# Kernel tuning notes

Hardware: AMD Instinct MI355X
Metric: run time of the kernel (lower is better)

## Reference

```python
import jax, jax.numpy as jnp
import numpy as np


def _segment_mean(x, idx, num_segments):
    # mean-aggregate rows of x into num_segments buckets (PyG SAGEConv default aggr)
    s = jax.ops.segment_sum(x, idx, num_segments=num_segments)
    c = jax.ops.segment_sum(jnp.ones((idx.shape[0],), x.dtype), idx, num_segments=num_segments)
    return s / jnp.maximum(c, 1.0)[:, None]


def setup_inputs() -> dict:
    key = jax.random.key(0)
    ks = jax.random.split(key, 12)
    N_LIG, N_PROT, D, H, E = 100000, 50000, 64, 128, 2000000
    sc = 0.05
    return {
        "x_lig": jax.random.normal(ks[0], (N_LIG, D), jnp.float32),
        "x_prot": jax.random.normal(ks[1], (N_PROT, D), jnp.float32),
        "W_l_lp": jax.random.normal(ks[2], (D, H), jnp.float32) * sc,
        "b_lp": jnp.zeros((H,), jnp.float32),
        "W_r_lp": jax.random.normal(ks[3], (D, H), jnp.float32) * sc,
        "W_l_pl": jax.random.normal(ks[4], (D, H), jnp.float32) * sc,
        "b_pl": jnp.zeros((H,), jnp.float32),
        "W_r_pl": jax.random.normal(ks[5], (D, H), jnp.float32) * sc,
        "W_lin": jax.random.normal(ks[6], (H, 1), jnp.float32) * sc,
        "b_lin": jnp.zeros((1,), jnp.float32),
        "src_lp": jax.random.randint(ks[7], (E,), 0, N_LIG, jnp.int32),
        "dst_lp": jax.random.randint(ks[8], (E,), 0, N_PROT, jnp.int32),
        "src_pl": jax.random.randint(ks[9], (E,), 0, N_PROT, jnp.int32),
        "dst_pl": jax.random.randint(ks[10], (E,), 0, N_LIG, jnp.int32),
    }


def reference(x_lig, x_prot, W_l_lp, b_lp, W_r_lp, W_l_pl, b_pl, W_r_pl,
              W_lin, b_lin, src_lp, dst_lp, src_pl, dst_pl):
    n_lig = x_lig.shape[0]
    n_prot = x_prot.shape[0]
    # SAGEConv ('ligand','interacts','protein'): gather ligand feats along edges, mean into proteins
    agg_prot = _segment_mean(x_lig[src_lp], dst_lp, n_prot)          # [N_prot, D]
    h_prot = jax.nn.relu(agg_prot @ W_l_lp + b_lp + x_prot @ W_r_lp)  # [N_prot, H] (dead downstream, as in original)
    # SAGEConv ('protein','interacts','ligand')
    agg_lig = _segment_mean(x_prot[src_pl], dst_pl, n_lig)           # [N_lig, D]
    h_lig = jax.nn.relu(agg_lig @ W_l_pl + b_pl + x_lig @ W_r_pl)    # [N_lig, H]
    ligand_out = h_lig.mean(axis=0)                                  # [H]
    del h_prot  # original computes it but never uses it (only 'ligand' feeds the head)
    return ligand_out @ W_lin + b_lin                                # [1]
```

## Files before the change

### kernel.cpp

```cpp
#include <hip/hip_runtime.h>

#define D 64
#define H 128
#define BN 128
#define CAP 3456
#define NBB 256
#define CE 7816

typedef short bf16x8 __attribute__((ext_vector_type(8)));
typedef float f32x4  __attribute__((ext_vector_type(4)));
typedef float f32x2  __attribute__((ext_vector_type(2)));

__device__ __forceinline__ ushort f2bf(float f) {
    unsigned u = __float_as_uint(f);
    unsigned r = (u + 0x7FFFu + ((u >> 16) & 1u)) >> 16;
    return (ushort)r;
}

__device__ __forceinline__ bf16x8 pack8v(f32x4 a, f32x4 b) {
    ushort o[8];
    o[0]=f2bf(a[0]); o[1]=f2bf(a[1]); o[2]=f2bf(a[2]); o[3]=f2bf(a[3]);
    o[4]=f2bf(b[0]); o[5]=f2bf(b[1]); o[6]=f2bf(b[2]); o[7]=f2bf(b[3]);
    bf16x8 r;
    __builtin_memcpy(&r, o, 16);
    return r;
}

__device__ __forceinline__ void acc16(f32x2* a, uint4 v) {
    a[0] += __builtin_amdgcn_cvt_pk_f32_fp8((int)v.x, false);
    a[1] += __builtin_amdgcn_cvt_pk_f32_fp8((int)v.x, true);
    a[2] += __builtin_amdgcn_cvt_pk_f32_fp8((int)v.y, false);
    a[3] += __builtin_amdgcn_cvt_pk_f32_fp8((int)v.y, true);
    a[4] += __builtin_amdgcn_cvt_pk_f32_fp8((int)v.z, false);
    a[5] += __builtin_amdgcn_cvt_pk_f32_fp8((int)v.z, true);
    a[6] += __builtin_amdgcn_cvt_pk_f32_fp8((int)v.w, false);
    a[7] += __builtin_amdgcn_cvt_pk_f32_fp8((int)v.w, true);
}

__device__ __forceinline__ unsigned pk4_fp8(float x0, float x1, float x2, float x3) {
    int w = __builtin_amdgcn_cvt_pk_fp8_f32(x0, x1, 0, false);
    w = __builtin_amdgcn_cvt_pk_fp8_f32(x2, x3, w, true);
    return (unsigned)w;
}

__device__ __forceinline__ int wave_incl_scan(int v, int lane) {
    #pragma unroll
    for (int o = 1; o < 64; o <<= 1) {
        int x = __shfl_up(v, o);
        if (lane >= o) v += x;
    }
    return v;
}

__global__ __launch_bounds__(256)
void stage1_kernel(const float* __restrict__ xp, unsigned char* __restrict__ xp8, int totalp,
                   const float* __restrict__ Wl, const float* __restrict__ Wr,
                   ushort* __restrict__ wprep,
                   const int* __restrict__ dst, int* __restrict__ cnt,
                   int E, int K, int ce, int PB) {
    __shared__ int scnt[800];
    int bid = blockIdx.x;
    int t = threadIdx.x;
    if (bid < PB) {
        int i = (bid * 256 + t) * 16;
        if (i < totalp) {
            const f32x4* p = (const f32x4*)(xp + i);
            f32x4 a = __builtin_nontemporal_load(p);
            f32x4 b = __builtin_nontemporal_load(p + 1);
            f32x4 c = __builtin_nontemporal_load(p + 2);
            f32x4 d = __builtin_nontemporal_load(p + 3);
            uint4 o;
            o.x = pk4_fp8(a[0], a[1], a[2], a[3]);
            o.y = pk4_fp8(b[0], b[1], b[2], b[3]);
            o.z = pk4_fp8(c[0], c[1], c[2], c[3]);
            o.w = pk4_fp8(d[0], d[1], d[2], d[3]);
            *(uint4*)(xp8 + i) = o;
        }
    } else if (bid < PB + 8) {
        int e = (bid - PB) * 256 + t;
        if (e < 2048) {
            int lane = e & 63;
            int ks = (e >> 6) & 3;
            int ht = e >> 8;
            int h = ht * 16 + (lane & 15);
            int kgp = lane >> 4;
            ushort o[8];
            #pragma unroll
            for (int j = 0; j < 8; ++j) {
                int k = (ks < 2) ? (kgp * 16 + ks * 8 + j)
                                 : (ks * 32 + kgp * 8 + j);
                float v = (k < D) ? Wl[k * H + h] : Wr[(k - D) * H + h];
                o[j] = f2bf(v);
            }
            *(bf16x8*)(wprep + (size_t)e * 8) = *(bf16x8*)o;
        }
    } else {
        int blk = bid - PB - 8;
        for (int b = t; b < 800; b += 256) scnt[b] = 0;
        __syncthreads();
        int e0 = blk * ce;
        int e1 = min(E, e0 + ce);
        for (int i = e0 + t * 4; i < e1; i += 1024) {
            int4 d4 = *(const int4*)(dst + i);
            atomicAdd(&scnt[d4.x >> 7], 1);
            atomicAdd(&scnt[d4.y >> 7], 1);
            atomicAdd(&scnt[d4.z >> 7], 1);
            atomicAdd(&scnt[d4.w >> 7], 1);
        }
        __syncthreads();
        int* row = cnt + (size_t)blk * K;
        for (int b = t; b < K; b += 256) row[b] = scnt[b];
    }
}

__global__ __launch_bounds__(NBB)
void part_scan_kernel(const int* __restrict__ cnt, int* __restrict__ off,
                      int* __restrict__ tot, int K) {
    __shared__ int wsum[NBB / 64];
    int b = blockIdx.x;
    int t = threadIdx.x;
    int lane = t & 63, wv = t >> 6;
    int v = cnt[(size_t)t * K + b];
    int incl = wave_incl_scan(v, lane);
    if (lane == 63) wsum[wv] = incl;
    __syncthreads();
    int add = 0;
    #pragma unroll
    for (int w = 0; w < NBB / 64; ++w)
        if (w < wv) add += wsum[w];
    off[(size_t)t * K + b] = incl + add - v;
    if (t == NBB - 1) tot[b] = incl + add;
}

__global__ __launch_bounds__(512)
void part_scatter_kernel(const int* __restrict__ src, const int* __restrict__ dst,
                         const int* __restrict__ off, int* __restrict__ gb,
                         int E, int K, int ce) {
    __shared__ int shist[800];
    __shared__ int sbase[800];
    __shared__ int gdelta[800];
    __shared__ int lcur[800];
    __shared__ int sscan[512];
    __shared__ int ebuf[CE];
    __shared__ unsigned short bkt[CE];

    int blk = blockIdx.x, t = threadIdx.x;
    int e0 = blk * ce;
    int e1 = min(E, e0 + ce);
    int myn = e1 - e0;

    int4 dreg[4];
    #pragma unroll
    for (int k = 0; k < 4; ++k) {
        int i = e0 + (t + k * 512) * 4;
        dreg[k] = (i < e1) ? *(const int4*)(dst + i) : make_int4(-1, -1, -1, -1);
    }

    for (int b = t; b < 800; b += 512) shist[b] = 0;
    __syncthreads();
    #pragma unroll
    for (int k = 0; k < 4; ++k) {
        if (dreg[k].x >= 0) {
            atomicAdd(&shist[dreg[k].x >> 7], 1);
            atomicAdd(&shist[dreg[k].y >> 7], 1);
            atomicAdd(&shist[dreg[k].z >> 7], 1);
            atomicAdd(&shist[dreg[k].w >> 7], 1);
        }
    }
    __syncthreads();
    int c0 = 0, c1 = 0;
    if (t < 400) { c0 = shist[2 * t]; c1 = shist[2 * t + 1]; }
    int cs = c0 + c1;
    sscan[t] = (t < 400) ? cs : 0;
    __syncthreads();
    for (int o = 1; o < 512; o <<= 1) {
        int x = (t >= o) ? sscan[t - o] : 0;
        __syncthreads();
        sscan[t] += x;
        __syncthreads();
    }
    if (t < 400) {
        int ex = sscan[t] - cs;
        sbase[2 * t] = ex;
        sbase[2 * t + 1] = ex + c0;
    }
    __syncthreads();
    const int* orow = off + (size_t)blk * K;
    for (int b = t; b < K; b += 512) {
        int sb = sbase[b];
        gdelta[b] = orow[b] - sb;
        lcur[b] = sb;
    }
    __syncthreads();
    #pragma unroll
    for (int k = 0; k < 4; ++k) {
        int i = e0 + (t + k * 512) * 4;
        if (dreg[k].x >= 0) {
            int4 s4 = *(const int4*)(src + i);
            int b, p;
            b = dreg[k].x >> 7; p = atomicAdd(&lcur[b], 1);
            ebuf[p] = (s4.x & 0xFFFF) | ((dreg[k].x & 127) << 16); bkt[p] = (unsigned short)b;
            b = dreg[k].y >> 7; p = atomicAdd(&lcur[b], 1);
            ebuf[p] = (s4.y & 0xFFFF) | ((dreg[k].y & 127) << 16); bkt[p] = (unsigned short)b;
            b = dreg[k].z >> 7; p = atomicAdd(&lcur[b], 1);
            ebuf[p] = (s4.z & 0xFFFF) | ((dreg[k].z & 127) << 16); bkt[p] = (unsigned short)b;
            b = dreg[k].w >> 7; p = atomicAdd(&lcur[b], 1);
            ebuf[p] = (s4.w & 0xFFFF) | ((dreg[k].w & 127) << 16); bkt[p] = (unsigned short)b;
        }
    }
    __syncthreads();
    for (int p = t; p < myn; p += 512) {
        int b = bkt[p];
        int loc = gdelta[b] + p;
        if (loc < CAP) gb[(size_t)b * CAP + loc] = ebuf[p];
    }
}

__global__ __launch_bounds__(512, 6)
void fused_kernel(const unsigned char* __restrict__ xp8, const float* __restrict__ x_lig,
                  const int* __restrict__ gtot, const int* __restrict__ gb,
                  const ushort* __restrict__ wprep, const float* __restrict__ bvec,
                  float* __restrict__ pgrid, int N) {
    __shared__ int sdeg[BN];
    __shared__ int sstart[BN];
    __shared__ int scur[BN];
    __shared__ int swtot[2];
    __shared__ int scsr[CAP];
    __shared__ float sred[8][H];

    int b = blockIdx.x, t = threadIdx.x;
    int wv = t >> 6, lane = t & 63;
    int cnt = min(gtot[b], CAP);
    const int* mygb = gb + (size_t)b * CAP;

    int ev[7];
    #pragma unroll
    for (int k = 0; k < 7; ++k) {
        int i = t + k * 512;
        ev[k] = (i < cnt) ? __builtin_nontemporal_load(&mygb[i]) : -1;
    }

    if (t < BN) sdeg[t] = 0;
    __syncthreads();
    #pragma unroll
    for (int k = 0; k < 7; ++k)
        if (ev[k] >= 0) atomicAdd(&sdeg[ev[k] >> 16], 1);
    __syncthreads();
    int degv = 0, inclv = 0;
    if (t < BN) {
        degv = sdeg[t];
        inclv = wave_incl_scan(degv, lane);
        if (lane == 63) swtot[wv] = inclv;
    }
    __syncthreads();
    if (t < BN) {
        int ex = inclv + ((t >= 64) ? swtot[0] : 0) - degv;
        sstart[t] = ex;
        scur[t] = ex;
    }
    __syncthreads();
    #pragma unroll
    for (int k = 0; k < 7; ++k)
        if (ev[k] >= 0) {
            int p = atomicAdd(&scur[ev[k] >> 16], 1);
            scsr[p] = ev[k] & 0xFFFF;
        }
    __syncthreads();

    int r = lane & 15, kg = lane >> 4;

    int grow = b * BN + wv * 16 + r;
    f32x4 va = {0.f,0.f,0.f,0.f}, vb = va, vc = va, vd = va;
    if (grow < N) {
        const f32x4* xr = (const f32x4*)(x_lig + (size_t)grow * D);
        va = __builtin_nontemporal_load(xr + kg * 2);
        vb = __builtin_nontemporal_load(xr + kg * 2 + 1);
        vc = __builtin_nontemporal_load(xr + 8 + kg * 2);
        vd = __builtin_nontemporal_load(xr + 8 + kg * 2 + 1);
    }

    int ln = wv * 16 + r;
    int s0 = sstart[ln], dg = sdeg[ln];
    f32x2 a[8];
    #pragma unroll
    for (int k = 0; k < 8; ++k) { a[k][0] = 0.f; a[k][1] = 0.f; }
    int j = 0;
    for (; j + 1 < dg; j += 2) {
        int i0 = scsr[s0 + j];
        int i1 = scsr[s0 + j + 1];
        uint4 v0 = *((const uint4*)(xp8 + (size_t)i0 * D) + kg);
        uint4 v1 = *((const uint4*)(xp8 + (size_t)i1 * D) + kg);
        acc16(a, v0);
        acc16(a, v1);
    }
    if (j < dg) {
        int i0 = scsr[s0 + j];
        uint4 v0 = *((const uint4*)(xp8 + (size_t)i0 * D) + kg);
        acc16(a, v0);
    }

    float inv = 1.0f / fmaxf((float)dg, 1.0f);
    ushort o0[8], o1[8];
    #pragma unroll
    for (int k = 0; k < 4; ++k) {
        o0[2*k]   = f2bf(a[k][0] * inv);
        o0[2*k+1] = f2bf(a[k][1] * inv);
        o1[2*k]   = f2bf(a[4+k][0] * inv);
        o1[2*k+1] = f2bf(a[4+k][1] * inv);
    }
    bf16x8 A0, A1;
    __builtin_memcpy(&A0, o0, 16);
    __builtin_memcpy(&A1, o1, 16);

    bf16x8 A2 = pack8v(va, vb);
    bf16x8 A3 = pack8v(vc, vd);

    float hsum[8];
    bool full = (b * BN + wv * 16 + 16 <= N);
    const bf16x8* wp = (const bf16x8*)wprep;
    #pragma unroll 2
    for (int ht = 0; ht < 8; ++ht) {
        f32x4 acc = {0.f, 0.f, 0.f, 0.f};
        acc = __builtin_amdgcn_mfma_f32_16x16x32_bf16(A0, wp[(ht*4+0)*64 + lane], acc, 0, 0, 0);
        acc = __builtin_amdgcn_mfma_f32_16x16x32_bf16(A1, wp[(ht*4+1)*64 + lane], acc, 0, 0, 0);
        acc = __builtin_amdgcn_mfma_f32_16x16x32_bf16(A2, wp[(ht*4+2)*64 + lane], acc, 0, 0, 0);
        acc = __builtin_amdgcn_mfma_f32_16x16x32_bf16(A3, wp[(ht*4+3)*64 + lane], acc, 0, 0, 0);
        float bb = bvec[ht * 16 + r];
        float s = 0.f;
        if (full) {
            #pragma unroll
            for (int i = 0; i < 4; ++i) s += fmaxf(acc[i] + bb, 0.f);
        } else {
            #pragma unroll
            for (int i = 0; i < 4; ++i) {
                int row = b * BN + wv * 16 + kg * 4 + i;
                if (row < N) s += fmaxf(acc[i] + bb, 0.f);
            }
        }
        hsum[ht] = s;
    }

    #pragma unroll
    for (int ht = 0; ht < 8; ++ht) {
        float v = hsum[ht];
        v += __shfl_xor(v, 16);
        v += __shfl_xor(v, 32);
        if (lane < 16) sred[wv][ht * 16 + lane] = v;
    }
    __syncthreads();
    if (t < H) {
        float s = 0.f;
        #pragma unroll
        for (int w = 0; w < 8; ++w) s += sred[w][t];
        pgrid[(size_t)b * H + t] = s;
    }
}

__global__ __launch_bounds__(128)
void reduce1_kernel(const float* __restrict__ pgrid, int nb, float* __restrict__ pgrid2) {
    int t = threadIdx.x;
    float s = 0.f;
    for (int r = blockIdx.x; r < nb; r += 64) s += pgrid[(size_t)r * H + t];
    pgrid2[(size_t)blockIdx.x * H + t] = s;
}

__global__ __launch_bounds__(128)
void head_kernel(const float* __restrict__ pgrid2,
                 const float* __restrict__ W_lin, const float* __restrict__ b_lin,
                 float* __restrict__ out, float invN) {
    __shared__ float sh[H];
    int t = threadIdx.x;
    float s = 0.f;
    #pragma unroll 8
    for (int r = 0; r < 64; ++r) s += pgrid2[(size_t)r * H + t];
    sh[t] = s * invN * W_lin[t];
    __syncthreads();
    if (t == 0) {
        float tot = b_lin[0];
        for (int i = 0; i < H; ++i) tot += sh[i];
        out[0] = tot;
    }
}

extern "C" void kernel_launch(void* const* d_in, const int* in_sizes, int n_in,
                              void* d_out, int out_size, void* d_ws, size_t ws_size,
                              hipStream_t stream) {
    const float* x_lig  = (const float*)d_in[0];
    const float* x_prot = (const float*)d_in[1];
    const float* W_l_pl = (const float*)d_in[5];
    const float* b_pl   = (const float*)d_in[6];
    const float* W_r_pl = (const float*)d_in[7];
    const float* W_lin  = (const float*)d_in[8];
    const float* b_lin  = (const float*)d_in[9];
    const int*   src_pl = (const int*)d_in[12];
    const int*   dst_pl = (const int*)d_in[13];

    int N  = in_sizes[0] / D;
    int NP = in_sizes[1] / D;
    int E  = in_sizes[12];
    int K  = (N + BN - 1) / BN;

    char* base = (char*)d_ws;
    unsigned char* xp8 = (unsigned char*)base; base += (size_t)NP * D;
    float* pgrid  = (float*)base;   base += (size_t)K * H * sizeof(float);
    float* pgrid2 = (float*)base;   base += (size_t)64 * H * sizeof(float);
    ushort* wprep = (ushort*)base;  base += (size_t)2048 * 8 * sizeof(ushort);
    int* cnt      = (int*)base;     base += (size_t)NBB * K * sizeof(int);
    int* off      = (int*)base;     base += (size_t)NBB * K * sizeof(int);
    int* tot      = (int*)base;     base += (size_t)K * sizeof(int);
    base = (char*)(((size_t)base + 255) & ~(size_t)255);
    int* gb       = (int*)base;     base += (size_t)K * CAP * sizeof(int);

    int ce = ((E + NBB - 1) / NBB + 3) & ~3;
    int PB = (NP * D / 16 + 255) / 256;

    stage1_kernel<<<PB + 8 + NBB, 256, 0, stream>>>(x_prot, xp8, NP * D,
                                                    W_l_pl, W_r_pl, wprep,
                                                    dst_pl, cnt, E, K, ce, PB);
    part_scan_kernel<<<K, NBB, 0, stream>>>(cnt, off, tot, K);
    part_scatter_kernel<<<NBB, 512, 0, stream>>>(src_pl, dst_pl, off, gb, E, K, ce);
    fused_kernel<<<K, 512, 0, stream>>>(xp8, x_lig, tot, gb, wprep, b_pl, pgrid, N);
    reduce1_kernel<<<64, 128, 0, stream>>>(pgrid, K, pgrid2);
    head_kernel<<<1, 128, 0, stream>>>(pgrid2, W_lin, b_lin, (float*)d_out,
                                       1.0f / (float)N);
}
```

Before: 79.26 us.

## Sort nodes by degree within block and stage weights in LDS

Each block computes a rank of its 128 destination nodes by in-degree and remaps the rows so each wave's 16 lanes handle nodes of similar degree, which reduces divergence in the gather loop. The prepacked weight fragments are also copied into shared memory once per block and read from LDS in the MFMA loop instead of global memory. The cost is an O(BN) rank loop per thread, an extra 32KB of LDS that may lower occupancy, and a row mask for tail handling.

```diff
diff --git a/kernel.cpp b/kernel.cpp
--- a/kernel.cpp
+++ b/kernel.cpp
@@ -225,14 +225,24 @@
     __shared__ int sstart[BN];
     __shared__ int scur[BN];
     __shared__ int swtot[2];
+    __shared__ int slot[BN];
     __shared__ int scsr[CAP];
     __shared__ float sred[8][H];
+    __shared__ ushort swp[2048 * 8];
 
     int b = blockIdx.x, t = threadIdx.x;
     int wv = t >> 6, lane = t & 63;
     int cnt = min(gtot[b], CAP);
     const int* mygb = gb + (size_t)b * CAP;
 
+    {
+        const uint4* wsrc = (const uint4*)wprep;
+        uint4* wdst = (uint4*)swp;
+        #pragma unroll
+        for (int k = 0; k < 4; ++k)
+            wdst[t + k * 512] = wsrc[t + k * 512];
+    }
+
     int ev[7];
     #pragma unroll
     for (int k = 0; k < 7; ++k) {
@@ -246,17 +256,22 @@
     for (int k = 0; k < 7; ++k)
         if (ev[k] >= 0) atomicAdd(&sdeg[ev[k] >> 16], 1);
     __syncthreads();
-    int degv = 0, inclv = 0;
+    int degv = 0, inclv = 0, rk = 0;
     if (t < BN) {
         degv = sdeg[t];
         inclv = wave_incl_scan(degv, lane);
         if (lane == 63) swtot[wv] = inclv;
+        for (int jj = 0; jj < BN; ++jj) {
+            int dj = sdeg[jj];
+            rk += (dj > degv) || (dj == degv && jj < t);
+        }
     }
     __syncthreads();
     if (t < BN) {
         int ex = inclv + ((t >= 64) ? swtot[0] : 0) - degv;
         sstart[t] = ex;
         scur[t] = ex;
+        slot[rk] = t;
     }
     __syncthreads();
     #pragma unroll
@@ -269,17 +284,18 @@
 
     int r = lane & 15, kg = lane >> 4;
 
-    int grow = b * BN + wv * 16 + r;
+    int ln = slot[wv * 16 + r];
+    int node = b * BN + ln;
+
     f32x4 va = {0.f,0.f,0.f,0.f}, vb = va, vc = va, vd = va;
-    if (grow < N) {
-        const f32x4* xr = (const f32x4*)(x_lig + (size_t)grow * D);
+    if (node < N) {
+        const f32x4* xr = (const f32x4*)(x_lig + (size_t)node * D);
         va = __builtin_nontemporal_load(xr + kg * 2);
         vb = __builtin_nontemporal_load(xr + kg * 2 + 1);
         vc = __builtin_nontemporal_load(xr + 8 + kg * 2);
         vd = __builtin_nontemporal_load(xr + 8 + kg * 2 + 1);
     }
 
-    int ln = wv * 16 + r;
     int s0 = sstart[ln], dg = sdeg[ln];
     f32x2 a[8];
     #pragma unroll
@@ -315,28 +331,32 @@
     bf16x8 A2 = pack8v(va, vb);
     bf16x8 A3 = pack8v(vc, vd);
 
+    bool full = (b * BN + BN <= N);
+    int vmask = 15;
+    if (!full) {
+        vmask = 0;
+        #pragma unroll
+        for (int i = 0; i < 4; ++i)
+            if (b * BN + slot[wv * 16 + kg * 4 + i] < N) vmask |= 1 << i;
+    }
+
     float hsum[8];
-    bool full = (b * BN + wv * 16 + 16 <= N);
-    const bf16x8* wp = (const bf16x8*)wprep;
     #pragma unroll 2
     for (int ht = 0; ht < 8; ++ht) {
         f32x4 acc = {0.f, 0.f, 0.f, 0.f};
-        acc = __builtin_amdgcn_mfma_f32_16x16x32_bf16(A0, wp[(ht*4+0)*64 + lane], acc, 0, 0, 0);
-        acc = __builtin_amdgcn_mfma_f32_16x16x32_bf16(A1, wp[(ht*4+1)*64 + lane], acc, 0, 0, 0);
-        acc = __builtin_amdgcn_mfma_f32_16x16x32_bf16(A2, wp[(ht*4+2)*64 + lane], acc, 0, 0, 0);
-        acc = __builtin_amdgcn_mfma_f32_16x16x32_bf16(A3, wp[(ht*4+3)*64 + lane], acc, 0, 0, 0);
+        const bf16x8* w0 = (const bf16x8*)(swp + ((ht*4+0)*64 + lane)*8);
+        const bf16x8* w1 = (const bf16x8*)(swp + ((ht*4+1)*64 + lane)*8);
+        const bf16x8* w2 = (const bf16x8*)(swp + ((ht*4+2)*64 + lane)*8);
+        const bf16x8* w3 = (const bf16x8*)(swp + ((ht*4+3)*64 + lane)*8);
+        acc = __builtin_amdgcn_mfma_f32_16x16x32_bf16(A0, *w0, acc, 0, 0, 0);
+        acc = __builtin_amdgcn_mfma_f32_16x16x32_bf16(A1, *w1, acc, 0, 0, 0);
+        acc = __builtin_amdgcn_mfma_f32_16x16x32_bf16(A2, *w2, acc, 0, 0, 0);
+        acc = __builtin_amdgcn_mfma_f32_16x16x32_bf16(A3, *w3, acc, 0, 0, 0);
         float bb = bvec[ht * 16 + r];
         float s = 0.f;
-        if (full) {
-            #pragma unroll
-            for (int i = 0; i < 4; ++i) s += fmaxf(acc[i] + bb, 0.f);
-        } else {
-            #pragma unroll
-            for (int i = 0; i < 4; ++i) {
-                int row = b * BN + wv * 16 + kg * 4 + i;
-                if (row < N) s += fmaxf(acc[i] + bb, 0.f);
-            }
-        }
+        #pragma unroll
+        for (int i = 0; i < 4; ++i)
+            if ((vmask >> i) & 1) s += fmaxf(acc[i] + bb, 0.f);
         hsum[ht] = s;
     }
 
```

Result: no change. 80.71 us (+1.8%).

## Split fused kernel into CSR build and gather-MFMA kernels

Applied to the files above, without the earlier changes.

Splits the fused per-block kernel in two. The first kernel sorts bucketed edges into a per-block CSR of 16-bit source indices in global memory, plus packed start/degree metadata. The second kernel reads that CSR from global memory, gathers the fp8 protein rows, and runs the MFMA head. Freeing the large shared CSR array and raising launch bounds to 8 blocks per CU aims at higher occupancy for the latency-bound gather, at the cost of an extra launch and a global round-trip for the CSR.

```diff
diff --git a/kernel.cpp b/kernel.cpp
--- a/kernel.cpp
+++ b/kernel.cpp
@@ -216,17 +216,14 @@
     }
 }
 
-__global__ __launch_bounds__(512, 6)
-void fused_kernel(const unsigned char* __restrict__ xp8, const float* __restrict__ x_lig,
-                  const int* __restrict__ gtot, const int* __restrict__ gb,
-                  const ushort* __restrict__ wprep, const float* __restrict__ bvec,
-                  float* __restrict__ pgrid, int N) {
+__global__ __launch_bounds__(512, 8)
+void csr_build_kernel(const int* __restrict__ gtot, const int* __restrict__ gb,
+                      ushort* __restrict__ gcsr, int* __restrict__ gmeta) {
     __shared__ int sdeg[BN];
     __shared__ int sstart[BN];
     __shared__ int scur[BN];
     __shared__ int swtot[2];
-    __shared__ int scsr[CAP];
-    __shared__ float sred[8][H];
+    __shared__ ushort scsr[CAP];
 
     int b = blockIdx.x, t = threadIdx.x;
     int wv = t >> 6, lane = t & 63;
@@ -263,38 +260,46 @@
     for (int k = 0; k < 7; ++k)
         if (ev[k] >= 0) {
             int p = atomicAdd(&scur[ev[k] >> 16], 1);
-            scsr[p] = ev[k] & 0xFFFF;
-        }
-    __syncthreads();
-
+            scsr[p] = (ushort)(ev[k] & 0xFFFF);
+        }
+    __syncthreads();
+
+    ushort* out = gcsr + (size_t)b * CAP;
+    for (int i = t; i < cnt; i += 512) out[i] = scsr[i];
+    if (t < BN) gmeta[b * BN + t] = (sstart[t] << 16) | sdeg[t];
+}
+
+__global__ __launch_bounds__(512, 8)
+void gather_mfma_kernel(const unsigned char* __restrict__ xp8,
+                        const float* __restrict__ x_lig,
+                        const ushort* __restrict__ gcsr, const int* __restrict__ gmeta,
+                        const ushort* __restrict__ wprep, const float* __restrict__ bvec,
+                        float* __restrict__ pgrid, int N) {
+    __shared__ float sred[8][H];
+
+    int b = blockIdx.x, t = threadIdx.x;
+    int wv = t >> 6, lane = t & 63;
     int r = lane & 15, kg = lane >> 4;
 
-    int grow = b * BN + wv * 16 + r;
-    f32x4 va = {0.f,0.f,0.f,0.f}, vb = va, vc = va, vd = va;
-    if (grow < N) {
-        const f32x4* xr = (const f32x4*)(x_lig + (size_t)grow * D);
-        va = __builtin_nontemporal_load(xr + kg * 2);
-        vb = __builtin_nontemporal_load(xr + kg * 2 + 1);
-        vc = __builtin_nontemporal_load(xr + 8 + kg * 2);
-        vd = __builtin_nontemporal_load(xr + 8 + kg * 2 + 1);
-    }
-
     int ln = wv * 16 + r;
-    int s0 = sstart[ln], dg = sdeg[ln];
+    int meta = gmeta[b * BN + ln];
+    int s0 = meta >> 16, dg = meta & 0xFFFF;
+    const ushort* csr = gcsr + (size_t)b * CAP;
+
     f32x2 a[8];
     #pragma unroll
     for (int k = 0; k < 8; ++k) { a[k][0] = 0.f; a[k][1] = 0.f; }
     int j = 0;
     for (; j + 1 < dg; j += 2) {
-        int i0 = scsr[s0 + j];
-        int i1 = scsr[s0 + j + 1];
+        int i0 = csr[s0 + j];
+        int i1 = csr[s0 + j + 1];
         uint4 v0 = *((const uint4*)(xp8 + (size_t)i0 * D) + kg);
         uint4 v1 = *((const uint4*)(xp8 + (size_t)i1 * D) + kg);
         acc16(a, v0);
         acc16(a, v1);
     }
     if (j < dg) {
-        int i0 = scsr[s0 + j];
+        int i0 = csr[s0 + j];
         uint4 v0 = *((const uint4*)(xp8 + (size_t)i0 * D) + kg);
         acc16(a, v0);
     }
@@ -312,8 +317,20 @@
     __builtin_memcpy(&A0, o0, 16);
     __builtin_memcpy(&A1, o1, 16);
 
-    bf16x8 A2 = pack8v(va, vb);
-    bf16x8 A3 = pack8v(vc, vd);
+    int grow = b * BN + ln;
+    bf16x8 A2, A3;
+    if (grow < N) {
+        const f32x4* xr = (const f32x4*)(x_lig + (size_t)grow * D);
+        f32x4 va = __builtin_nontemporal_load(xr + kg * 2);
+        f32x4 vb = __builtin_nontemporal_load(xr + kg * 2 + 1);
+        A2 = pack8v(va, vb);
+        f32x4 vc = __builtin_nontemporal_load(xr + 8 + kg * 2);
+        f32x4 vd = __builtin_nontemporal_load(xr + 8 + kg * 2 + 1);
+        A3 = pack8v(vc, vd);
+    } else {
+        A2 = bf16x8{0,0,0,0,0,0,0,0};
+        A3 = A2;
+    }
 
     float hsum[8];
     bool full = (b * BN + wv * 16 + 16 <= N);
@@ -408,8 +425,10 @@
     int* cnt      = (int*)base;     base += (size_t)NBB * K * sizeof(int);
     int* off      = (int*)base;     base += (size_t)NBB * K * sizeof(int);
     int* tot      = (int*)base;     base += (size_t)K * sizeof(int);
+    int* gmeta    = (int*)base;     base += (size_t)K * BN * sizeof(int);
     base = (char*)(((size_t)base + 255) & ~(size_t)255);
     int* gb       = (int*)base;     base += (size_t)K * CAP * sizeof(int);
+    ushort* gcsr  = (ushort*)base;  base += (size_t)K * CAP * sizeof(ushort);
 
     int ce = ((E + NBB - 1) / NBB + 3) & ~3;
     int PB = (NP * D / 16 + 255) / 256;
@@ -419,7 +438,9 @@
                                                     dst_pl, cnt, E, K, ce, PB);
     part_scan_kernel<<<K, NBB, 0, stream>>>(cnt, off, tot, K);
     part_scatter_kernel<<<NBB, 512, 0, stream>>>(src_pl, dst_pl, off, gb, E, K, ce);
-    fused_kernel<<<K, 512, 0, stream>>>(xp8, x_lig, tot, gb, wprep, b_pl, pgrid, N);
+    csr_build_kernel<<<K, 512, 0, stream>>>(tot, gb, gcsr, gmeta);
+    gather_mfma_kernel<<<K, 512, 0, stream>>>(xp8, x_lig, gcsr, gmeta, wprep, b_pl,
+                                              pgrid, N);
     reduce1_kernel<<<64, 128, 0, stream>>>(pgrid, K, pgrid2);
     head_kernel<<<1, 128, 0, stream>>>(pgrid2, W_lin, b_lin, (float*)d_out,
                                        1.0f / (float)N);
```

Measured after the change: 86.64 us. 9.3% more time.
